# Performance work log

Hardware: AMD Instinct MI355X
Metric: run time of the kernel (lower is better)

Reference implementation:

```python
import jax, jax.numpy as jnp
import numpy as np

N, NPER, B, E = 65536, 1024, 64, 1048576
IN_F, HID, K, NCLS = 128, 64, 16, 10


def setup_inputs() -> dict:
    key = jax.random.key(0)
    ks = jax.random.split(key, 12)
    x = jax.random.normal(ks[0], (N, IN_F), jnp.float32)
    # block-structured intra-graph edges: 64 graphs of 1024 contiguous nodes
    gid = jax.random.randint(ks[1], (E,), 0, B)
    src = gid * NPER + jax.random.randint(ks[2], (E,), 0, NPER)
    dst = gid * NPER + jax.random.randint(ks[3], (E,), 0, NPER)
    edge_index = jnp.stack([src, dst]).astype(jnp.int32)
    batch = (jnp.arange(N, dtype=jnp.int32) // NPER).astype(jnp.int32)
    def lin(k, fo, fi):
        kw, kb = jax.random.split(k)
        s = 1.0 / np.sqrt(fi)
        return (jax.random.uniform(kw, (fo, fi), jnp.float32, -s, s),
                jax.random.uniform(kb, (fo,), jnp.float32, -s, s))
    W1, b1 = lin(ks[4], HID, IN_F)
    W2, b2 = lin(ks[5], HID, HID)
    Wp, bp = lin(ks[6], K, HID)      # DMoN cluster-assignment MLP (single Linear)
    Wl, bl = lin(ks[7], NCLS, HID)   # final classifier
    return {"x": x, "edge_index": edge_index, "batch": batch,
            "W1": W1, "b1": b1, "W2": W2, "b2": b2,
            "Wp": Wp, "bp": bp, "Wl": Wl, "bl": bl}


def gcn_conv(x, src, dst, W, b):
    # GCNConv with add_self_loops=True, symmetric normalization
    n = x.shape[0]
    deg = jax.ops.segment_sum(jnp.ones(src.shape[0], x.dtype), dst,
                              num_segments=n) + 1.0  # +1 for self-loop
    dinv = jax.lax.rsqrt(deg)
    h = x @ W.T
    coef = (dinv[src] * dinv[dst])[:, None]
    agg = jax.ops.segment_sum(h[src] * coef, dst, num_segments=n)
    agg = agg + h * (dinv * dinv)[:, None]  # self-loop contribution
    return agg + b


def reference(x, edge_index, batch, W1, b1, W2, b2, Wp, bp, Wl, bl):
    src, dst = edge_index[0], edge_index[1]
    h = jax.nn.relu(gcn_conv(x, src, dst, W1, b1))
    h = jax.nn.relu(gcn_conv(h, src, dst, W2, b2))
    # to_dense_batch: graphs are equal-sized and contiguous -> reshape, mask all True
    Xb = h.reshape(B, NPER, HID)
    # DMoN cluster assignment (dropout=0.0, mask all ones)
    s = jax.nn.softmax(Xb @ Wp.T + bp, axis=-1)          # [B, NPER, K]
    Xp = jax.nn.selu(jnp.einsum('bnk,bnh->bkh', s, Xb))   # pooled clusters [B, K, HID]
    out = Xp.mean(axis=1)                                  # [B, HID]
    logits = out @ Wl.T + bl                               # [B, NCLS]
    return logits
```

## Files before the change

### kernel.cpp

```cpp
#include <hip/hip_runtime.h>
#include <cstddef>

#define N_NODES 65536
#define NPER    1024
#define NGRAPH  64
#define HID     64
#define IN_F    128
#define KCLUS   16
#define NCLS    10
#define ECAP    18432

__global__ __launch_bounds__(256) void bucket_kernel(const int* __restrict__ src,
                                                     const int* __restrict__ dst,
                                                     int* __restrict__ ecnt,
                                                     int* __restrict__ gedges, int E) {
    __shared__ int hist[NGRAPH];
    __shared__ int base_l[NGRAPH];
    const int t = threadIdx.x;
    const int e0 = blockIdx.x * 1024;
    if (t < NGRAPH) hist[t] = 0;
    __syncthreads();

    int gg[4], rr[4], pk[4];
#pragma unroll
    for (int i = 0; i < 4; ++i) {
        int idx = e0 + i * 256 + t;
        if (idx < E) {
            int d = dst[idx], s = src[idx];
            int g = d >> 10;
            gg[i] = g;
            pk[i] = ((d & 1023) << 10) | (s & 1023);
            rr[i] = atomicAdd(&hist[g], 1);
        } else gg[i] = -1;
    }
    __syncthreads();
    if (t < NGRAPH) base_l[t] = atomicAdd(&ecnt[t], hist[t]);
    __syncthreads();
#pragma unroll
    for (int i = 0; i < 4; ++i) {
        if (gg[i] >= 0) {
            int pos = base_l[gg[i]] + rr[i];
            if (pos < ECAP) gedges[gg[i] * ECAP + pos] = pk[i];
        }
    }
}

__global__ __launch_bounds__(1024) void csr_kernel(const int* __restrict__ gedges,
                                                   const int* __restrict__ ecnt,
                                                   int* __restrict__ rp,
                                                   unsigned short* __restrict__ esorted,
                                                   float* __restrict__ dinv) {
    __shared__ int hist[NPER];
    __shared__ int ts[NPER];
    const int g = blockIdx.x, t = threadIdx.x;
    const int ec = ecnt[g];
    const int* ge = gedges + (size_t)g * ECAP;

    hist[t] = 0;
    __syncthreads();
    for (int i = t; i < ec; i += 1024) atomicAdd(&hist[ge[i] >> 10], 1);
    __syncthreads();

    const int h0 = hist[t];
    ts[t] = h0;
    __syncthreads();
    for (int off = 1; off < 1024; off <<= 1) {
        int x = (t >= off) ? ts[t - off] : 0;
        __syncthreads();
        ts[t] += x;
        __syncthreads();
    }
    const int excl = ts[t] - h0;

    rp[g * (NPER + 1) + t] = excl;
    if (t == NPER - 1) rp[g * (NPER + 1) + NPER] = ts[t];
    dinv[g * NPER + t] = rsqrtf((float)h0 + 1.0f);

    hist[t] = excl;
    __syncthreads();

    unsigned short* es = esorted + (size_t)g * ECAP;
    for (int i = t; i < ec; i += 1024) {
        int pk = ge[i];
        int pos = atomicAdd(&hist[pk >> 10], 1);
        es[pos] = (unsigned short)(pk & 1023);
    }
}

template <int K>
__global__ __launch_bounds__(256) void linear_kernel(const float* __restrict__ X,
                                                     const float* __restrict__ W,
                                                     float* __restrict__ Y) {
    __shared__ float xsT[64][68];
    __shared__ float wsT[64][68];
    const int t = threadIdx.x;
    const size_t row0 = (size_t)blockIdx.x * 64;
    const int r0 = (t >> 4) * 4;
    const int c0 = (t & 15) * 4;
    float acc[4][4] = {};

    for (int kc = 0; kc < K; kc += 64) {
        __syncthreads();
        for (int i = t; i < 1024; i += 256) {
            int row = i >> 4, k4 = (i & 15) << 2;
            float4 v = *(const float4*)(X + (row0 + row) * K + kc + k4);
            xsT[k4 + 0][row] = v.x;
            xsT[k4 + 1][row] = v.y;
            xsT[k4 + 2][row] = v.z;
            xsT[k4 + 3][row] = v.w;
        }
        for (int i = t; i < 1024; i += 256) {
            int col = i >> 4, k4 = (i & 15) << 2;
            float4 v = *(const float4*)(W + col * K + kc + k4);
            wsT[k4 + 0][col] = v.x;
            wsT[k4 + 1][col] = v.y;
            wsT[k4 + 2][col] = v.z;
            wsT[k4 + 3][col] = v.w;
        }
        __syncthreads();

#pragma unroll 8
        for (int k = 0; k < 64; ++k) {
            float4 xv = *(const float4*)&xsT[k][r0];
            float4 wv = *(const float4*)&wsT[k][c0];
            acc[0][0] = fmaf(xv.x, wv.x, acc[0][0]);
            acc[0][1] = fmaf(xv.x, wv.y, acc[0][1]);
            acc[0][2] = fmaf(xv.x, wv.z, acc[0][2]);
            acc[0][3] = fmaf(xv.x, wv.w, acc[0][3]);
            acc[1][0] = fmaf(xv.y, wv.x, acc[1][0]);
            acc[1][1] = fmaf(xv.y, wv.y, acc[1][1]);
            acc[1][2] = fmaf(xv.y, wv.z, acc[1][2]);
            acc[1][3] = fmaf(xv.y, wv.w, acc[1][3]);
            acc[2][0] = fmaf(xv.z, wv.x, acc[2][0]);
            acc[2][1] = fmaf(xv.z, wv.y, acc[2][1]);
            acc[2][2] = fmaf(xv.z, wv.z, acc[2][2]);
            acc[2][3] = fmaf(xv.z, wv.w, acc[2][3]);
            acc[3][0] = fmaf(xv.w, wv.x, acc[3][0]);
            acc[3][1] = fmaf(xv.w, wv.y, acc[3][1]);
            acc[3][2] = fmaf(xv.w, wv.z, acc[3][2]);
            acc[3][3] = fmaf(xv.w, wv.w, acc[3][3]);
        }
    }

#pragma unroll
    for (int i = 0; i < 4; ++i) {
        float4 v = make_float4(acc[i][0], acc[i][1], acc[i][2], acc[i][3]);
        *(float4*)(Y + (row0 + r0 + i) * HID + c0) = v;
    }
}

__global__ __launch_bounds__(512) void agg_kernel(const float* __restrict__ h,
                                                  const unsigned short* __restrict__ esorted,
                                                  const int* __restrict__ rp,
                                                  const float* __restrict__ dinv,
                                                  const float* __restrict__ bias,
                                                  float* __restrict__ outp) {
    __shared__ float Hs[8][NPER + 1];
    __shared__ float dl[NPER];
    const int g = blockIdx.x >> 3;
    const int f0 = (blockIdx.x & 7) * 8;
    const int t = threadIdx.x;
    const int base = g * NPER;

    for (int r = t; r < NPER; r += 512) {
        const float* hp = h + (size_t)(base + r) * HID + f0;
        float4 a = *(const float4*)hp;
        float4 b = *(const float4*)(hp + 4);
        float dv = dinv[base + r];
        dl[r] = dv;
        Hs[0][r] = a.x * dv; Hs[1][r] = a.y * dv; Hs[2][r] = a.z * dv; Hs[3][r] = a.w * dv;
        Hs[4][r] = b.x * dv; Hs[5][r] = b.y * dv; Hs[6][r] = b.z * dv; Hs[7][r] = b.w * dv;
    }
    float bb[8];
#pragma unroll
    for (int j = 0; j < 8; ++j) bb[j] = bias[f0 + j];
    const unsigned short* es = esorted + (size_t)g * ECAP;
    const int* rpg = rp + g * (NPER + 1);
    __syncthreads();

    for (int ld = t; ld < NPER; ld += 512) {
        int p = rpg[ld];
        const int pe = rpg[ld + 1];
        float acc[8];
#pragma unroll
        for (int j = 0; j < 8; ++j) acc[j] = Hs[j][ld];
        for (; p < pe; ++p) {
            int sl = es[p];
#pragma unroll
            for (int j = 0; j < 8; ++j) acc[j] += Hs[j][sl];
        }
        const float dv = dl[ld];
        float4 o0, o1;
        o0.x = fmaxf(fmaf(acc[0], dv, bb[0]), 0.f);
        o0.y = fmaxf(fmaf(acc[1], dv, bb[1]), 0.f);
        o0.z = fmaxf(fmaf(acc[2], dv, bb[2]), 0.f);
        o0.w = fmaxf(fmaf(acc[3], dv, bb[3]), 0.f);
        o1.x = fmaxf(fmaf(acc[4], dv, bb[4]), 0.f);
        o1.y = fmaxf(fmaf(acc[5], dv, bb[5]), 0.f);
        o1.z = fmaxf(fmaf(acc[6], dv, bb[6]), 0.f);
        o1.w = fmaxf(fmaf(acc[7], dv, bb[7]), 0.f);
        float* op = outp + (size_t)(base + ld) * HID + f0;
        *(float4*)op = o0;
        *(float4*)(op + 4) = o1;
    }
}

__global__ __launch_bounds__(256) void pool1_kernel(const float* __restrict__ h,
                                                    const float* __restrict__ Wp,
                                                    const float* __restrict__ bp,
                                                    float* __restrict__ xpart) {
    __shared__ float xs[128][HID + 1];
    __shared__ float ss[128][KCLUS + 1];
    __shared__ float wp[KCLUS][HID];
    __shared__ float bps[KCLUS];
    const int g = blockIdx.x >> 3;
    const int c = blockIdx.x & 7;
    const int t = threadIdx.x;
    const float* hb = h + ((size_t)g * NPER + c * 128) * HID;

    for (int i = t; i < 128 * HID / 4; i += 256) {
        float4 v = ((const float4*)hb)[i];
        int row = i >> 4, col = (i & 15) * 4;
        xs[row][col] = v.x; xs[row][col + 1] = v.y; xs[row][col + 2] = v.z; xs[row][col + 3] = v.w;
    }
    for (int i = t; i < KCLUS * HID; i += 256) wp[i >> 6][i & 63] = Wp[i];
    if (t < KCLUS) bps[t] = bp[t];
    __syncthreads();

    if (t < 128) {
        float lg[KCLUS];
        float mx = -1e30f;
#pragma unroll
        for (int k = 0; k < KCLUS; ++k) {
            float a = bps[k];
#pragma unroll 8
            for (int hh = 0; hh < HID; ++hh) a = fmaf(xs[t][hh], wp[k][hh], a);
            lg[k] = a;
            mx = fmaxf(mx, a);
        }
        float sum = 0.f;
#pragma unroll
        for (int k = 0; k < KCLUS; ++k) {
            lg[k] = __expf(lg[k] - mx);
            sum += lg[k];
        }
        float inv = 1.0f / sum;
#pragma unroll
        for (int k = 0; k < KCLUS; ++k) ss[t][k] = lg[k] * inv;
    }
    __syncthreads();

    const int hcol = t & 63;
    const int k0 = (t >> 6) * 4;
    float a0 = 0.f, a1 = 0.f, a2 = 0.f, a3 = 0.f;
#pragma unroll 8
    for (int n = 0; n < 128; ++n) {
        float xv = xs[n][hcol];
        a0 = fmaf(ss[n][k0 + 0], xv, a0);
        a1 = fmaf(ss[n][k0 + 1], xv, a1);
        a2 = fmaf(ss[n][k0 + 2], xv, a2);
        a3 = fmaf(ss[n][k0 + 3], xv, a3);
    }
    float* xp = xpart + (((size_t)(g * 8 + c)) * KCLUS + k0) * HID + hcol;
    xp[0] = a0; xp[HID] = a1; xp[2 * HID] = a2; xp[3 * HID] = a3;
}

__global__ __launch_bounds__(256) void pool2_kernel(const float* __restrict__ xpart,
                                                    const float* __restrict__ Wl,
                                                    const float* __restrict__ bl,
                                                    float* __restrict__ out) {
    __shared__ float xp[KCLUS][HID + 1];
    __shared__ float outm[HID];
    const int g = blockIdx.x;
    const int t = threadIdx.x;
    const int hcol = t & 63;
    const int k0 = (t >> 6) * 4;
    const float* base = xpart + (size_t)g * 8 * KCLUS * HID;

    float a[4] = {};
#pragma unroll
    for (int c = 0; c < 8; ++c)
#pragma unroll
        for (int j = 0; j < 4; ++j)
            a[j] += base[(c * KCLUS + k0 + j) * HID + hcol];

    const float sc = 1.0507009873554805f, al = 1.6732632423543772f;
#pragma unroll
    for (int j = 0; j < 4; ++j) {
        float v = a[j];
        xp[k0 + j][hcol] = v > 0.f ? sc * v : sc * al * (__expf(v) - 1.f);
    }
    __syncthreads();

    if (t < HID) {
        float m = 0.f;
#pragma unroll
        for (int k = 0; k < KCLUS; ++k) m += xp[k][t];
        outm[t] = m * (1.0f / KCLUS);
    }
    __syncthreads();

    if (t < NCLS) {
        float acc = bl[t];
#pragma unroll 8
        for (int hh = 0; hh < HID; ++hh) acc = fmaf(outm[hh], Wl[t * HID + hh], acc);
        out[g * NCLS + t] = acc;
    }
}

extern "C" void kernel_launch(void* const* d_in, const int* in_sizes, int n_in,
                              void* d_out, int out_size, void* d_ws, size_t ws_size,
                              hipStream_t stream) {
    const float* x  = (const float*)d_in[0];
    const int* eidx = (const int*)d_in[1];
    const float* W1 = (const float*)d_in[3];
    const float* b1 = (const float*)d_in[4];
    const float* W2 = (const float*)d_in[5];
    const float* b2 = (const float*)d_in[6];
    const float* Wp = (const float*)d_in[7];
    const float* bp = (const float*)d_in[8];
    const float* Wl = (const float*)d_in[9];
    const float* bl = (const float*)d_in[10];
    float* out = (float*)d_out;

    const int E = in_sizes[1] / 2;
    const int* src = eidx;
    const int* dst = eidx + E;

    char* w = (char*)d_ws;
    int*            ecnt    = (int*)w;            w += 256;
    int*            gedges  = (int*)w;            w += (size_t)NGRAPH * ECAP * 4;
    unsigned short* esorted = (unsigned short*)w; w += (size_t)NGRAPH * ECAP * 2;
    int*            rp      = (int*)w;            w += (size_t)NGRAPH * (NPER + 1) * 4;
    float*          dinv    = (float*)w;          w += (size_t)N_NODES * 4;
    float*          A       = (float*)w;          w += (size_t)N_NODES * HID * 4;
    float*          Bf      = (float*)w;          w += (size_t)N_NODES * HID * 4;
    float*          xpart   = (float*)w;          w += (size_t)NGRAPH * 8 * KCLUS * HID * 4;

    hipMemsetAsync(ecnt, 0, 256, stream);
    bucket_kernel<<<(E + 1023) / 1024, 256, 0, stream>>>(src, dst, ecnt, gedges, E);
    csr_kernel<<<NGRAPH, 1024, 0, stream>>>(gedges, ecnt, rp, esorted, dinv);

    linear_kernel<IN_F><<<N_NODES / 64, 256, 0, stream>>>(x, W1, A);
    agg_kernel<<<NGRAPH * 8, 512, 0, stream>>>(A, esorted, rp, dinv, b1, Bf);

    linear_kernel<HID><<<N_NODES / 64, 256, 0, stream>>>(Bf, W2, A);
    agg_kernel<<<NGRAPH * 8, 512, 0, stream>>>(A, esorted, rp, dinv, b2, Bf);

    pool1_kernel<<<NGRAPH * 8, 256, 0, stream>>>(Bf, Wp, bp, xpart);
    pool2_kernel<<<NGRAPH, 256, 0, stream>>>(xpart, Wl, bl, out);
}
```

Measured before the change: 256.8 us.

## Use row-major padded LDS layout in aggregation and fuse pooling kernels

The aggregation kernel now stores each node's 8 features contiguously in shared memory with a padded stride of 12. This lets each gathered neighbor be read as two float4 loads instead of eight scalar loads from separate arrays. Separately, the two pooling kernels are merged into one: the last block of each graph, found through an atomic counter, does the final reduction, SELU and classifier, which removes one kernel launch. The padded stride may bring back LDS bank conflicts, and the fusion adds an atomic plus thread fences.

```diff
diff --git a/kernel.cpp b/kernel.cpp
--- a/kernel.cpp
+++ b/kernel.cpp
@@ -9,6 +9,7 @@
 #define KCLUS   16
 #define NCLS    10
 #define ECAP    18432
+#define HSTRIDE 12
 
 __global__ __launch_bounds__(256) void bucket_kernel(const int* __restrict__ src,
                                                      const int* __restrict__ dst,
@@ -155,7 +156,7 @@
                                                   const float* __restrict__ dinv,
                                                   const float* __restrict__ bias,
                                                   float* __restrict__ outp) {
-    __shared__ float Hs[8][NPER + 1];
+    __shared__ float Hs[NPER * HSTRIDE];
     __shared__ float dl[NPER];
     const int g = blockIdx.x >> 3;
     const int f0 = (blockIdx.x & 7) * 8;
@@ -168,8 +169,9 @@
         float4 b = *(const float4*)(hp + 4);
         float dv = dinv[base + r];
         dl[r] = dv;
-        Hs[0][r] = a.x * dv; Hs[1][r] = a.y * dv; Hs[2][r] = a.z * dv; Hs[3][r] = a.w * dv;
-        Hs[4][r] = b.x * dv; Hs[5][r] = b.y * dv; Hs[6][r] = b.z * dv; Hs[7][r] = b.w * dv;
+        float* row = &Hs[r * HSTRIDE];
+        *(float4*)row = make_float4(a.x * dv, a.y * dv, a.z * dv, a.w * dv);
+        *(float4*)(row + 4) = make_float4(b.x * dv, b.y * dv, b.z * dv, b.w * dv);
     }
     float bb[8];
 #pragma unroll
@@ -181,38 +183,47 @@
     for (int ld = t; ld < NPER; ld += 512) {
         int p = rpg[ld];
         const int pe = rpg[ld + 1];
-        float acc[8];
-#pragma unroll
-        for (int j = 0; j < 8; ++j) acc[j] = Hs[j][ld];
+        const float* srow = &Hs[ld * HSTRIDE];
+        float4 acc0 = *(const float4*)srow;
+        float4 acc1 = *(const float4*)(srow + 4);
         for (; p < pe; ++p) {
-            int sl = es[p];
-#pragma unroll
-            for (int j = 0; j < 8; ++j) acc[j] += Hs[j][sl];
+            const float* rw = &Hs[(int)es[p] * HSTRIDE];
+            float4 a = *(const float4*)rw;
+            float4 b = *(const float4*)(rw + 4);
+            acc0.x += a.x; acc0.y += a.y; acc0.z += a.z; acc0.w += a.w;
+            acc1.x += b.x; acc1.y += b.y; acc1.z += b.z; acc1.w += b.w;
         }
         const float dv = dl[ld];
         float4 o0, o1;
-        o0.x = fmaxf(fmaf(acc[0], dv, bb[0]), 0.f);
-        o0.y = fmaxf(fmaf(acc[1], dv, bb[1]), 0.f);
-        o0.z = fmaxf(fmaf(acc[2], dv, bb[2]), 0.f);
-        o0.w = fmaxf(fmaf(acc[3], dv, bb[3]), 0.f);
-        o1.x = fmaxf(fmaf(acc[4], dv, bb[4]), 0.f);
-        o1.y = fmaxf(fmaf(acc[5], dv, bb[5]), 0.f);
-        o1.z = fmaxf(fmaf(acc[6], dv, bb[6]), 0.f);
-        o1.w = fmaxf(fmaf(acc[7], dv, bb[7]), 0.f);
+        o0.x = fmaxf(fmaf(acc0.x, dv, bb[0]), 0.f);
+        o0.y = fmaxf(fmaf(acc0.y, dv, bb[1]), 0.f);
+        o0.z = fmaxf(fmaf(acc0.z, dv, bb[2]), 0.f);
+        o0.w = fmaxf(fmaf(acc0.w, dv, bb[3]), 0.f);
+        o1.x = fmaxf(fmaf(acc1.x, dv, bb[4]), 0.f);
+        o1.y = fmaxf(fmaf(acc1.y, dv, bb[5]), 0.f);
+        o1.z = fmaxf(fmaf(acc1.z, dv, bb[6]), 0.f);
+        o1.w = fmaxf(fmaf(acc1.w, dv, bb[7]), 0.f);
         float* op = outp + (size_t)(base + ld) * HID + f0;
         *(float4*)op = o0;
         *(float4*)(op + 4) = o1;
     }
 }
 
-__global__ __launch_bounds__(256) void pool1_kernel(const float* __restrict__ h,
-                                                    const float* __restrict__ Wp,
-                                                    const float* __restrict__ bp,
-                                                    float* __restrict__ xpart) {
+__global__ __launch_bounds__(256) void pool_kernel(const float* __restrict__ h,
+                                                   const float* __restrict__ Wp,
+                                                   const float* __restrict__ bp,
+                                                   const float* __restrict__ Wl,
+                                                   const float* __restrict__ bl,
+                                                   float* __restrict__ xpart,
+                                                   int* __restrict__ pcnt,
+                                                   float* __restrict__ out) {
     __shared__ float xs[128][HID + 1];
     __shared__ float ss[128][KCLUS + 1];
     __shared__ float wp[KCLUS][HID];
     __shared__ float bps[KCLUS];
+    __shared__ float xp[KCLUS][HID + 1];
+    __shared__ float outm[HID];
+    __shared__ int amlast;
     const int g = blockIdx.x >> 3;
     const int c = blockIdx.x & 7;
     const int t = threadIdx.x;
@@ -261,28 +272,23 @@
         a2 = fmaf(ss[n][k0 + 2], xv, a2);
         a3 = fmaf(ss[n][k0 + 3], xv, a3);
     }
-    float* xp = xpart + (((size_t)(g * 8 + c)) * KCLUS + k0) * HID + hcol;
-    xp[0] = a0; xp[HID] = a1; xp[2 * HID] = a2; xp[3 * HID] = a3;
-}
-
-__global__ __launch_bounds__(256) void pool2_kernel(const float* __restrict__ xpart,
-                                                    const float* __restrict__ Wl,
-                                                    const float* __restrict__ bl,
-                                                    float* __restrict__ out) {
-    __shared__ float xp[KCLUS][HID + 1];
-    __shared__ float outm[HID];
-    const int g = blockIdx.x;
-    const int t = threadIdx.x;
-    const int hcol = t & 63;
-    const int k0 = (t >> 6) * 4;
-    const float* base = xpart + (size_t)g * 8 * KCLUS * HID;
-
+    float* xpw = xpart + (((size_t)(g * 8 + c)) * KCLUS + k0) * HID + hcol;
+    xpw[0] = a0; xpw[HID] = a1; xpw[2 * HID] = a2; xpw[3 * HID] = a3;
+
+    __threadfence();
+    __syncthreads();
+    if (t == 0) amlast = (atomicAdd(&pcnt[g], 1) == 7) ? 1 : 0;
+    __syncthreads();
+    if (!amlast) return;
+    __threadfence();
+
+    const float* basep = xpart + (size_t)g * 8 * KCLUS * HID;
     float a[4] = {};
 #pragma unroll
-    for (int c = 0; c < 8; ++c)
+    for (int cc = 0; cc < 8; ++cc)
 #pragma unroll
         for (int j = 0; j < 4; ++j)
-            a[j] += base[(c * KCLUS + k0 + j) * HID + hcol];
+            a[j] += basep[(cc * KCLUS + k0 + j) * HID + hcol];
 
     const float sc = 1.0507009873554805f, al = 1.6732632423543772f;
 #pragma unroll
@@ -329,6 +335,7 @@
 
     char* w = (char*)d_ws;
     int*            ecnt    = (int*)w;            w += 256;
+    int*            pcnt    = (int*)w;            w += 256;
     int*            gedges  = (int*)w;            w += (size_t)NGRAPH * ECAP * 4;
     unsigned short* esorted = (unsigned short*)w; w += (size_t)NGRAPH * ECAP * 2;
     int*            rp      = (int*)w;            w += (size_t)NGRAPH * (NPER + 1) * 4;
@@ -337,7 +344,7 @@
     float*          Bf      = (float*)w;          w += (size_t)N_NODES * HID * 4;
     float*          xpart   = (float*)w;          w += (size_t)NGRAPH * 8 * KCLUS * HID * 4;
 
-    hipMemsetAsync(ecnt, 0, 256, stream);
+    hipMemsetAsync(ecnt, 0, 512, stream);
     bucket_kernel<<<(E + 1023) / 1024, 256, 0, stream>>>(src, dst, ecnt, gedges, E);
     csr_kernel<<<NGRAPH, 1024, 0, stream>>>(gedges, ecnt, rp, esorted, dinv);
 
@@ -347,6 +354,5 @@
     linear_kernel<HID><<<N_NODES / 64, 256, 0, stream>>>(Bf, W2, A);
     agg_kernel<<<NGRAPH * 8, 512, 0, stream>>>(A, esorted, rp, dinv, b2, Bf);
 
-    pool1_kernel<<<NGRAPH * 8, 256, 0, stream>>>(Bf, Wp, bp, xpart);
-    pool2_kernel<<<NGRAPH, 256, 0, stream>>>(xpart, Wl, bl, out);
-}
+    pool_kernel<<<NGRAPH * 8, 256, 0, stream>>>(Bf, Wp, bp, Wl, bl, xpart, pcnt, out);
+}
```

Result: slower. 309.4 us (+20.5%).
